# Kernel tuning notes

Measured on AMD Instinct MI355X. Metric: run time of the kernel, lower is better.

Reference implementation:

```python
import jax, jax.numpy as jnp
import numpy as np

B, N, M, LDIM, RDIM, AGG = 4, 512, 512, 512, 512, 256


def setup_inputs() -> dict:
    key = jax.random.key(0)
    ks = jax.random.split(key, 7)
    data = jax.random.normal(ks[0], (B, N, LDIM), dtype=jnp.float32)
    crit = jax.random.normal(ks[1], (B, M, RDIM), dtype=jnp.float32)
    Wl = jax.random.normal(ks[2], (LDIM, AGG), dtype=jnp.float32) / np.sqrt(LDIM)
    bl = jax.random.normal(ks[3], (AGG,), dtype=jnp.float32) * 0.01
    Wr = jax.random.normal(ks[4], (RDIM, AGG), dtype=jnp.float32) / np.sqrt(RDIM)
    br = jax.random.normal(ks[5], (AGG,), dtype=jnp.float32) * 0.01
    agg = jax.random.uniform(ks[6], (AGG,), dtype=jnp.float32, minval=-0.01, maxval=0.01)
    return {"data": data, "crit": crit, "Wl": Wl, "bl": bl, "Wr": Wr, "br": br, "agg": agg}


def reference(data, crit, Wl, bl, Wr, br, agg):
    # linear projections
    datalin = jnp.einsum('bnl,la->bna', data, Wl) + bl   # [B,N,A]
    critlin = jnp.einsum('bmr,ra->bma', crit, Wr) + br   # [B,M,A]
    # broadcast add -> tanh -> reduce with agg vector: [B,N,M]
    linsum = jnp.tanh(datalin[:, :, None, :] + critlin[:, None, :, :])  # [B,N,M,A]
    dists = jnp.einsum('bnma,a->bnm', linsum, agg)
    return dists
```

## Files before the change

### kernel.cpp

```cpp
#include <hip/hip_runtime.h>


#define A_DIM 256
#define K_DIM 512
#define NROWS 2048

typedef unsigned short ushort;
typedef __attribute__((ext_vector_type(4))) unsigned short us4;

__device__ inline ushort f2bf(float x) {
    union { float f; unsigned u; } v; v.f = x;
    unsigned r = v.u + 0x7FFFu + ((v.u >> 16) & 1u);
    return (ushort)(r >> 16);
}
__device__ inline float bf2f(ushort h) {
    union { unsigned u; float f; } v; v.u = ((unsigned)h) << 16; return v.f;
}

__global__ __launch_bounds__(256) void proj_exp_kernel(
    const float* __restrict__ data, const float* __restrict__ crit,
    const float* __restrict__ Wl, const float* __restrict__ bl,
    const float* __restrict__ Wr, const float* __restrict__ br,
    ushort* __restrict__ ws16)
{
    __shared__ __align__(16) float Xs[16][68];
    __shared__ __align__(16) float Wsm[16][64];

    const int t   = threadIdx.x;
    const int bid = blockIdx.x;
    const int ct  = bid & 3;
    const int rt  = (bid >> 2) & 31;
    const int kh  = (bid >> 7) & 1;
    const int src = bid >> 8;

    const int r0 = rt * 64, c0 = ct * 64, kb = kh * 256;
    const float* X    = src ? crit : data;
    const float* W    = src ? Wr   : Wl;
    const float* bias = src ? br   : bl;
    ushort* ET = ws16 + (size_t)(src * 2 + kh) * ((size_t)A_DIM * NROWS);

    const int tx = t & 15;
    const int ty = t >> 4;
    const int sr = t >> 2;
    const int sk = (t & 3) * 4;
    const int wk = t >> 4;
    const int wc = (t & 15) * 4;

    float acc[4][4];
#pragma unroll
    for (int i = 0; i < 4; i++)
#pragma unroll
        for (int j = 0; j < 4; j++) acc[i][j] = 0.f;

    for (int k0 = 0; k0 < 256; k0 += 16) {
        float4 xv = *(const float4*)(X + (size_t)(r0 + sr) * K_DIM + kb + k0 + sk);
        float4 wv = *(const float4*)(W + (size_t)(kb + k0 + wk) * A_DIM + c0 + wc);
        __syncthreads();
        Xs[sk + 0][sr] = xv.x; Xs[sk + 1][sr] = xv.y;
        Xs[sk + 2][sr] = xv.z; Xs[sk + 3][sr] = xv.w;
        *(float4*)&Wsm[wk][wc] = wv;
        __syncthreads();
#pragma unroll
        for (int kk = 0; kk < 16; kk++) {
            float4 a4 = *(const float4*)&Xs[kk][ty * 4];
            float4 b4 = *(const float4*)&Wsm[kk][tx * 4];
            const float aa[4] = {a4.x, a4.y, a4.z, a4.w};
            const float bb[4] = {b4.x, b4.y, b4.z, b4.w};
#pragma unroll
            for (int i = 0; i < 4; i++)
#pragma unroll
                for (int j = 0; j < 4; j++)
                    acc[i][j] = fmaf(aa[i], bb[j], acc[i][j]);
        }
    }

    const float c2 = 2.8853900817779268f;
    float bvv[4] = {0.f, 0.f, 0.f, 0.f};
    if (kh == 0) {
        float4 bv = *(const float4*)(bias + c0 + tx * 4);
        bvv[0] = bv.x; bvv[1] = bv.y; bvv[2] = bv.z; bvv[3] = bv.w;
    }
#pragma unroll
    for (int j = 0; j < 4; j++) {
        us4 ev;
#pragma unroll
        for (int i = 0; i < 4; i++) {
            float v = (acc[i][j] + bvv[j]) * c2;
            v = fminf(fmaxf(v, -15.f), 15.f);
            ev[i] = f2bf(__builtin_amdgcn_exp2f(v));
        }
        *(us4*)(ET + (size_t)(c0 + tx * 4 + j) * NROWS + r0 + ty * 4) = ev;
    }
}

__global__ __launch_bounds__(256) void tanh_reduce_kernel(
    const ushort* __restrict__ ws16, const float* __restrict__ agg,
    float* __restrict__ out)
{
    __shared__ __align__(16) float et [64][34];
    __shared__ __align__(16) float ect[64][34];
    __shared__ float aggs[256];

    const int t   = threadIdx.x;
    const int bid = blockIdx.x;
    const int b   = bid >> 8;
    const int rem = bid & 255;
    const int n0  = (rem >> 4) * 32;
    const int m0  = (rem & 15) * 32;

    const size_t PLANE = (size_t)A_DIM * NROWS;
    const ushort* E1d = ws16;
    const ushort* E2d = ws16 + PLANE;
    const ushort* E1c = ws16 + 2 * PLANE;
    const ushort* E2c = ws16 + 3 * PLANE;
    const int row_n = b * 512 + n0;
    const int row_m = b * 512 + m0;

    const int tx = t & 15;
    const int ty = t >> 4;

    aggs[t] = 2.0f * agg[t];

    float acc00 = 0.f, acc01 = 0.f, acc10 = 0.f, acc11 = 0.f;
    float sagg = 0.f;

    for (int ch = 0; ch < 4; ch++) {
        const int a0 = ch * 64;
        __syncthreads();
#pragma unroll
        for (int rep = 0; rep < 2; rep++) {
            const int aL  = rep * 32 + (t >> 3);
            const int seg = (t & 7) * 4;
            const size_t offn = (size_t)(a0 + aL) * NROWS + row_n + seg;
            const size_t offm = (size_t)(a0 + aL) * NROWS + row_m + seg;
            us4 d1 = *(const us4*)(E1d + offn);
            us4 d2 = *(const us4*)(E2d + offn);
            us4 c1 = *(const us4*)(E1c + offm);
            us4 c2 = *(const us4*)(E2c + offm);
            float4 ev, cv;
            ev.x = bf2f(d1[0]) * bf2f(d2[0]); ev.y = bf2f(d1[1]) * bf2f(d2[1]);
            ev.z = bf2f(d1[2]) * bf2f(d2[2]); ev.w = bf2f(d1[3]) * bf2f(d2[3]);
            cv.x = bf2f(c1[0]) * bf2f(c2[0]); cv.y = bf2f(c1[1]) * bf2f(c2[1]);
            cv.z = bf2f(c1[2]) * bf2f(c2[2]); cv.w = bf2f(c1[3]) * bf2f(c2[3]);
            *(float4*)&et [aL][seg] = ev;
            *(float4*)&ect[aL][seg] = cv;
        }
        __syncthreads();

        for (int ap = 0; ap < 32; ap++) {
            const float2 ag = *(const float2*)&aggs[a0 + ap * 2];
            sagg += ag.x + ag.y;
            const float2 e0 = *(const float2*)&et [ap * 2 + 0][ty * 2];
            const float2 e1 = *(const float2*)&et [ap * 2 + 1][ty * 2];
            const float2 f0 = *(const float2*)&ect[ap * 2 + 0][tx * 2];
            const float2 f1 = *(const float2*)&ect[ap * 2 + 1][tx * 2];
            {
                float q0 = fmaf(e0.x, f0.x, 1.f), q1 = fmaf(e1.x, f1.x, 1.f);
                acc00 = fmaf(fmaf(ag.x, q1, ag.y * q0), __builtin_amdgcn_rcpf(q0 * q1), acc00);
            }
            {
                float q0 = fmaf(e0.x, f0.y, 1.f), q1 = fmaf(e1.x, f1.y, 1.f);
                acc01 = fmaf(fmaf(ag.x, q1, ag.y * q0), __builtin_amdgcn_rcpf(q0 * q1), acc01);
            }
            {
                float q0 = fmaf(e0.y, f0.x, 1.f), q1 = fmaf(e1.y, f1.x, 1.f);
                acc10 = fmaf(fmaf(ag.x, q1, ag.y * q0), __builtin_amdgcn_rcpf(q0 * q1), acc10);
            }
            {
                float q0 = fmaf(e0.y, f0.y, 1.f), q1 = fmaf(e1.y, f1.y, 1.f);
                acc11 = fmaf(fmaf(ag.x, q1, ag.y * q0), __builtin_amdgcn_rcpf(q0 * q1), acc11);
            }
        }
    }

    const float base = 0.5f * sagg;
    float2 r0v, r1v;
    r0v.x = base - acc00; r0v.y = base - acc01;
    r1v.x = base - acc10; r1v.y = base - acc11;
    float* o0 = out + ((size_t)(b * 512 + n0 + ty * 2) * 512) + m0 + tx * 2;
    *(float2*)o0         = r0v;
    *(float2*)(o0 + 512) = r1v;
}

extern "C" void kernel_launch(void* const* d_in, const int* in_sizes, int n_in,
                              void* d_out, int out_size, void* d_ws, size_t ws_size,
                              hipStream_t stream) {
    const float* data = (const float*)d_in[0];
    const float* crit = (const float*)d_in[1];
    const float* Wl   = (const float*)d_in[2];
    const float* bl   = (const float*)d_in[3];
    const float* Wr   = (const float*)d_in[4];
    const float* br   = (const float*)d_in[5];
    const float* agg  = (const float*)d_in[6];
    float* out  = (float*)d_out;
    ushort* ws16 = (ushort*)d_ws;

    proj_exp_kernel<<<dim3(512), 256, 0, stream>>>(data, crit, Wl, bl, Wr, br, ws16);

    tanh_reduce_kernel<<<dim3(1024), 256, 0, stream>>>(ws16, agg, out);
}
```

Baseline: 117.3 us.

## Enlarge tanh-reduce tiles to 64x64 with split-A partials and combine kernel

The tanh-reduce kernel now computes 64x64 output tiles with a 4x4 register block per thread instead of 32x32 with 2x2. This raises arithmetic reuse per shared-memory load. To keep enough blocks in flight, the A dimension is split into two halves that write separate partial outputs to workspace. A new combine kernel then sums the two halves. The cost is an extra launch, about 8 MB of extra global traffic, and more registers per thread.

```diff
diff --git a/kernel.cpp b/kernel.cpp
--- a/kernel.cpp
+++ b/kernel.cpp
@@ -95,18 +95,17 @@
 
 __global__ __launch_bounds__(256) void tanh_reduce_kernel(
     const ushort* __restrict__ ws16, const float* __restrict__ agg,
-    float* __restrict__ out)
+    float* __restrict__ partial)
 {
-    __shared__ __align__(16) float et [64][34];
-    __shared__ __align__(16) float ect[64][34];
-    __shared__ float aggs[256];
-
-    const int t   = threadIdx.x;
-    const int bid = blockIdx.x;
-    const int b   = bid >> 8;
-    const int rem = bid & 255;
-    const int n0  = (rem >> 4) * 32;
-    const int m0  = (rem & 15) * 32;
+    __shared__ __align__(16) float et [64][68];
+    __shared__ __align__(16) float ect[64][68];
+    __shared__ float aggs[128];
+
+    const int t    = threadIdx.x;
+    const int m0   = blockIdx.x * 64;
+    const int n0   = blockIdx.y * 64;
+    const int b    = blockIdx.z >> 1;
+    const int half = blockIdx.z & 1;
 
     const size_t PLANE = (size_t)A_DIM * NROWS;
     const ushort* E1d = ws16;
@@ -119,18 +118,24 @@
     const int tx = t & 15;
     const int ty = t >> 4;
 
-    aggs[t] = 2.0f * agg[t];
-
-    float acc00 = 0.f, acc01 = 0.f, acc10 = 0.f, acc11 = 0.f;
+    if (t < 128) aggs[t] = 2.0f * agg[half * 128 + t];
+
+    float acc[4][4];
+#pragma unroll
+    for (int i = 0; i < 4; i++)
+#pragma unroll
+        for (int j = 0; j < 4; j++) acc[i][j] = 0.f;
     float sagg = 0.f;
 
-    for (int ch = 0; ch < 4; ch++) {
-        const int a0 = ch * 64;
-        __syncthreads();
-#pragma unroll
-        for (int rep = 0; rep < 2; rep++) {
-            const int aL  = rep * 32 + (t >> 3);
-            const int seg = (t & 7) * 4;
+    const int aL = t >> 2;
+    const int qd = t & 3;
+
+    for (int ch = 0; ch < 2; ch++) {
+        const int a0 = half * 128 + ch * 64;
+        __syncthreads();
+#pragma unroll
+        for (int r = 0; r < 4; r++) {
+            const int seg = qd * 16 + r * 4;
             const size_t offn = (size_t)(a0 + aL) * NROWS + row_n + seg;
             const size_t offm = (size_t)(a0 + aL) * NROWS + row_m + seg;
             us4 d1 = *(const us4*)(E1d + offn);
@@ -147,39 +152,54 @@
         }
         __syncthreads();
 
-        for (int ap = 0; ap < 32; ap++) {
-            const float2 ag = *(const float2*)&aggs[a0 + ap * 2];
+        for (int p = 0; p < 32; p++) {
+            const float2 ag = *(const float2*)&aggs[ch * 64 + p * 2];
             sagg += ag.x + ag.y;
-            const float2 e0 = *(const float2*)&et [ap * 2 + 0][ty * 2];
-            const float2 e1 = *(const float2*)&et [ap * 2 + 1][ty * 2];
-            const float2 f0 = *(const float2*)&ect[ap * 2 + 0][tx * 2];
-            const float2 f1 = *(const float2*)&ect[ap * 2 + 1][tx * 2];
-            {
-                float q0 = fmaf(e0.x, f0.x, 1.f), q1 = fmaf(e1.x, f1.x, 1.f);
-                acc00 = fmaf(fmaf(ag.x, q1, ag.y * q0), __builtin_amdgcn_rcpf(q0 * q1), acc00);
-            }
-            {
-                float q0 = fmaf(e0.x, f0.y, 1.f), q1 = fmaf(e1.x, f1.y, 1.f);
-                acc01 = fmaf(fmaf(ag.x, q1, ag.y * q0), __builtin_amdgcn_rcpf(q0 * q1), acc01);
-            }
-            {
-                float q0 = fmaf(e0.y, f0.x, 1.f), q1 = fmaf(e1.y, f1.x, 1.f);
-                acc10 = fmaf(fmaf(ag.x, q1, ag.y * q0), __builtin_amdgcn_rcpf(q0 * q1), acc10);
-            }
-            {
-                float q0 = fmaf(e0.y, f0.y, 1.f), q1 = fmaf(e1.y, f1.y, 1.f);
-                acc11 = fmaf(fmaf(ag.x, q1, ag.y * q0), __builtin_amdgcn_rcpf(q0 * q1), acc11);
-            }
+            float4 e0 = *(const float4*)&et [p * 2 + 0][ty * 4];
+            float4 e1 = *(const float4*)&et [p * 2 + 1][ty * 4];
+            float4 f0 = *(const float4*)&ect[p * 2 + 0][tx * 4];
+            float4 f1 = *(const float4*)&ect[p * 2 + 1][tx * 4];
+            const float ea0[4] = {e0.x, e0.y, e0.z, e0.w};
+            const float ea1[4] = {e1.x, e1.y, e1.z, e1.w};
+            const float fa0[4] = {f0.x, f0.y, f0.z, f0.w};
+            const float fa1[4] = {f1.x, f1.y, f1.z, f1.w};
+#pragma unroll
+            for (int i = 0; i < 4; i++)
+#pragma unroll
+                for (int j = 0; j < 4; j++) {
+                    float q0 = fmaf(ea0[i], fa0[j], 1.f);
+                    float q1 = fmaf(ea1[i], fa1[j], 1.f);
+                    acc[i][j] = fmaf(fmaf(ag.x, q1, ag.y * q0),
+                                     __builtin_amdgcn_rcpf(q0 * q1), acc[i][j]);
+                }
         }
     }
 
     const float base = 0.5f * sagg;
-    float2 r0v, r1v;
-    r0v.x = base - acc00; r0v.y = base - acc01;
-    r1v.x = base - acc10; r1v.y = base - acc11;
-    float* o0 = out + ((size_t)(b * 512 + n0 + ty * 2) * 512) + m0 + tx * 2;
-    *(float2*)o0         = r0v;
-    *(float2*)(o0 + 512) = r1v;
+    float* pl = partial + (size_t)half * (1 << 20);
+#pragma unroll
+    for (int i = 0; i < 4; i++) {
+        float4 v;
+        v.x = base - acc[i][0]; v.y = base - acc[i][1];
+        v.z = base - acc[i][2]; v.w = base - acc[i][3];
+        *(float4*)(pl + ((size_t)(b * 512 + n0 + ty * 4 + i) * 512) + m0 + tx * 4) = v;
+    }
+}
+
+__global__ __launch_bounds__(256) void combine_kernel(
+    const float* __restrict__ partial, float* __restrict__ out)
+{
+    const int idx = blockIdx.x * 256 + threadIdx.x;
+    const float4* p0 = (const float4*)partial;
+    const float4* p1 = (const float4*)(partial + (1 << 20));
+    float4* o = (float4*)out;
+#pragma unroll
+    for (int r = 0; r < 2; r++) {
+        const int i = idx + r * 131072;
+        float4 a = p0[i], b = p1[i], v;
+        v.x = a.x + b.x; v.y = a.y + b.y; v.z = a.z + b.z; v.w = a.w + b.w;
+        o[i] = v;
+    }
 }
 
 extern "C" void kernel_launch(void* const* d_in, const int* in_sizes, int n_in,
@@ -192,10 +212,13 @@
     const float* Wr   = (const float*)d_in[4];
     const float* br   = (const float*)d_in[5];
     const float* agg  = (const float*)d_in[6];
-    float* out  = (float*)d_out;
+    float* out   = (float*)d_out;
     ushort* ws16 = (ushort*)d_ws;
+    float* wspart = (float*)((char*)d_ws + 4u * 1024u * 1024u);
 
     proj_exp_kernel<<<dim3(512), 256, 0, stream>>>(data, crit, Wl, bl, Wr, br, ws16);
 
-    tanh_reduce_kernel<<<dim3(1024), 256, 0, stream>>>(ws16, agg, out);
-}
+    tanh_reduce_kernel<<<dim3(8, 8, 8), 256, 0, stream>>>(ws16, agg, wspart);
+
+    combine_kernel<<<dim3(512), 256, 0, stream>>>(wspart, out);
+}
```

Result: no change. 118.8 us (+1.3%).
